# Optimization experiments

Hardware: AMD Instinct MI355X
Metric: run time of the kernel (lower is better)

The kernel has to match this reference:

```python
import jax, jax.numpy as jnp
import numpy as np

N, E, D, H, C, G = 50000, 800000, 128, 128, 16, 512


def setup_inputs() -> dict:
    key = jax.random.key(0)
    ks = jax.random.split(key, 8)

    def glorot(k, shape):
        lim = float(np.sqrt(6.0 / (shape[0] + shape[1])))
        return jax.random.uniform(k, shape, jnp.float32, -lim, lim)

    x = jax.random.normal(ks[0], (N, D), jnp.float32)
    edge_index = jax.random.randint(ks[1], (2, E), 0, N, dtype=jnp.int32)
    batch = jnp.sort(jax.random.randint(ks[2], (N,), 0, G, dtype=jnp.int32))
    return {
        'x': x,
        'edge_index': edge_index,
        'batch': batch,
        'W1': glorot(ks[3], (D, H)), 'b1': jnp.zeros((H,), jnp.float32),
        'W2': glorot(ks[4], (H, H)), 'b2': jnp.zeros((H,), jnp.float32),
        'lW1': glorot(ks[5], (4 * H, 2 * H)), 'lb1': jnp.zeros((2 * H,), jnp.float32),
        'lW2': glorot(ks[6], (2 * H, C)), 'lb2': jnp.zeros((C,), jnp.float32),
    }


def _gcn_norm(edge_index, n):
    # add self loops, then symmetric normalization D^-1/2 (A+I) D^-1/2
    loop = jnp.arange(n, dtype=edge_index.dtype)
    src = jnp.concatenate([edge_index[0], loop])
    dst = jnp.concatenate([edge_index[1], loop])
    ones = jnp.ones(src.shape[0], jnp.float32)
    deg = jax.ops.segment_sum(ones, dst, num_segments=n)
    dis = jnp.where(deg > 0, jax.lax.rsqrt(jnp.maximum(deg, 1.0)), 0.0)
    norm = dis[src] * dis[dst]  # [E+N]
    return src, dst, norm


def _gcn_conv(x, src, dst, norm, W, b, n):
    h = x @ W                                   # [N, H] transform first (PyG order)
    msg = h[src] * norm[:, None]                # gather + normalize, [E+N, H]
    out = jax.ops.segment_sum(msg, dst, num_segments=n)  # scatter-add
    return out + b


def _pool(x, batch, g):
    cnt = jax.ops.segment_sum(jnp.ones(x.shape[0], x.dtype), batch, num_segments=g)
    mean = jax.ops.segment_sum(x, batch, num_segments=g) / jnp.maximum(cnt, 1.0)[:, None]
    mx = jax.ops.segment_max(x, batch, num_segments=g)
    mx = jnp.where(cnt[:, None] > 0, mx, 0.0)
    return mean, mx


def reference(x, edge_index, batch, W1, b1, W2, b2, lW1, lb1, lW2, lb2):
    n = x.shape[0]
    src, dst, norm = _gcn_norm(edge_index, n)
    x0 = jax.nn.relu(_gcn_conv(x, src, dst, norm, W1, b1, n))   # dropout=identity (eval)
    g0_mean, g0_max = _pool(x0, batch, G)
    x1 = jax.nn.relu(_gcn_conv(x0, src, dst, norm, W2, b2, n))
    g1_mean, g1_max = _pool(x1, batch, G)
    g = jnp.concatenate([g0_mean, g0_max, g1_mean, g1_max], axis=-1)  # [G, 4H]
    h = jax.nn.relu(g @ lW1 + lb1)
    return h @ lW2 + lb2  # [G, C]
```

## Files before the change

### kernel.cpp

```cpp
#include <hip/hip_runtime.h>
#include <hip/hip_bf16.h>

#define NN 50000
#define EE 800000
#define DD 128
#define HH 128
#define CC 16
#define GG 512
#define NBLK_SCAN 196
#define NPAD 50176
#define GEMM_BLOCKS 782

typedef __attribute__((ext_vector_type(8))) short short8v;
typedef __attribute__((ext_vector_type(8))) unsigned short ushort8v;
typedef __attribute__((ext_vector_type(4))) float f32x4;

__device__ inline unsigned short f2bf(float x) {
    unsigned int u = __float_as_uint(x);
    u += 0x7fffu + ((u >> 16) & 1u);
    return (unsigned short)(u >> 16);
}

__global__ __launch_bounds__(256) void k_deg(const int* __restrict__ ei, int* __restrict__ deg) {
    int e = blockIdx.x * 256 + threadIdx.x;
    if (e < EE) atomicAdd(&deg[ei[EE + e]], 1);
}

__global__ __launch_bounds__(256) void k_scan1(const int* __restrict__ deg,
                                               int* __restrict__ offs, int* __restrict__ bsum,
                                               float* __restrict__ dis) {
    __shared__ int tmp[256];
    int i = blockIdx.x * 256 + threadIdx.x;
    int v = (i < NN) ? deg[i] : 0;
    if (i < NN) dis[i] = rsqrtf((float)v + 1.0f);
    tmp[threadIdx.x] = v;
    __syncthreads();
    for (int off = 1; off < 256; off <<= 1) {
        int t = (threadIdx.x >= off) ? tmp[threadIdx.x - off] : 0;
        __syncthreads();
        tmp[threadIdx.x] += t;
        __syncthreads();
    }
    if (i < NN) offs[i] = tmp[threadIdx.x] - v;
    if (threadIdx.x == 255) bsum[blockIdx.x] = tmp[255];
}

__global__ __launch_bounds__(256) void k_scan2(int* __restrict__ bsum) {
    __shared__ int tmp[256];
    int v = (threadIdx.x < NBLK_SCAN) ? bsum[threadIdx.x] : 0;
    tmp[threadIdx.x] = v;
    __syncthreads();
    for (int off = 1; off < 256; off <<= 1) {
        int t = (threadIdx.x >= off) ? tmp[threadIdx.x - off] : 0;
        __syncthreads();
        tmp[threadIdx.x] += t;
        __syncthreads();
    }
    bsum[threadIdx.x] = tmp[threadIdx.x] - v;
}

__global__ __launch_bounds__(256) void k_scan3(int* __restrict__ offs, const int* __restrict__ bsum,
                                               int* __restrict__ cursor) {
    int i = blockIdx.x * 256 + threadIdx.x;
    if (i < NN) {
        int v = offs[i] + bsum[blockIdx.x];
        offs[i] = v;
        cursor[i] = v;
    }
}

__global__ __launch_bounds__(256) void k_fill(const int* __restrict__ ei, const float* __restrict__ dis,
                                              int* __restrict__ cursor, unsigned int* __restrict__ adj) {
    int e = blockIdx.x * 256 + threadIdx.x;
    if (e >= EE) return;
    int s = ei[e];
    int d = ei[EE + e];
    int pos = atomicAdd(&cursor[d], 1);
    adj[pos] = ((unsigned int)s << 16) | (unsigned int)f2bf(dis[s] * dis[d]);
}

__global__ __launch_bounds__(256) void k_wfrag(const float* __restrict__ W1, const float* __restrict__ W2,
                                               unsigned short* __restrict__ Wf) {
    const float* W = blockIdx.x ? W2 : W1;
    unsigned short* o = Wf + blockIdx.x * 16384;
    for (int idx = threadIdx.x; idx < 2048; idx += 256) {
        int lane = idx & 63, ct = (idx >> 6) & 7, kt = idx >> 9;
        int col = ct * 16 + (lane & 15);
        int k0 = kt * 32 + (lane >> 4) * 8;
        ushort8v v;
        #pragma unroll
        for (int j = 0; j < 8; ++j) v[j] = f2bf(W[(k0 + j) * 128 + col]);
        *(ushort8v*)(o + idx * 8) = v;
    }
}

__global__ __launch_bounds__(256) void k_gemm(const float* __restrict__ Af,
                                              const unsigned short* __restrict__ Ab,
                                              const unsigned short* __restrict__ Wf,
                                              unsigned short* __restrict__ O,
                                              int af32) {
    __shared__ unsigned short Wl[16384];
    #pragma unroll
    for (int idx = threadIdx.x; idx < 2048; idx += 256)
        *(ushort8v*)(Wl + idx * 8) = *(const ushort8v*)(Wf + idx * 8);
    __syncthreads();

    int wid = threadIdx.x >> 6, lane = threadIdx.x & 63;
    int b = lane >> 4;
    int row = blockIdx.x * 64 + wid * 16 + (lane & 15);

    short8v a[4];
    if (af32) {
        int r = min(row, NN - 1);
        const float* ap = Af + (size_t)r * 128 + b * 8;
        #pragma unroll
        for (int kt = 0; kt < 4; ++kt) {
            float4 f0 = *(const float4*)(ap + kt * 32);
            float4 f1 = *(const float4*)(ap + kt * 32 + 4);
            short8v v;
            v[0] = (short)f2bf(f0.x); v[1] = (short)f2bf(f0.y);
            v[2] = (short)f2bf(f0.z); v[3] = (short)f2bf(f0.w);
            v[4] = (short)f2bf(f1.x); v[5] = (short)f2bf(f1.y);
            v[6] = (short)f2bf(f1.z); v[7] = (short)f2bf(f1.w);
            a[kt] = v;
        }
    } else {
        const unsigned short* ap = Ab + (size_t)row * 128 + b * 8;
        #pragma unroll
        for (int kt = 0; kt < 4; ++kt) a[kt] = *(const short8v*)(ap + kt * 32);
    }

    f32x4 z = 0.0f;
    f32x4 acc[8] = {z, z, z, z, z, z, z, z};
    #pragma unroll
    for (int kt = 0; kt < 4; ++kt) {
        #pragma unroll
        for (int ct = 0; ct < 8; ++ct) {
            short8v bfrag = *(const short8v*)(Wl + ((kt * 8 + ct) * 64 + lane) * 8);
            acc[ct] = __builtin_amdgcn_mfma_f32_16x16x32_bf16(a[kt], bfrag, acc[ct], 0, 0, 0);
        }
    }

    int orow = blockIdx.x * 64 + wid * 16 + b * 4;
    unsigned short* op = O + (size_t)orow * 128 + (lane & 15);
    #pragma unroll
    for (int j = 0; j < 4; ++j) {
        #pragma unroll
        for (int ct = 0; ct < 8; ++ct)
            op[(size_t)j * 128 + ct * 16] = f2bf(acc[ct][j]);
    }
}

__global__ __launch_bounds__(256) void k_conv(const unsigned short* __restrict__ h,
                                              const unsigned int* __restrict__ adj,
                                              const int* __restrict__ row_start,
                                              const int* __restrict__ deg,
                                              const float* __restrict__ dis,
                                              const float* __restrict__ bias,
                                              const int* __restrict__ batch,
                                              unsigned short* __restrict__ xout,
                                              float* __restrict__ gsum,
                                              float* __restrict__ gmax,
                                              float* __restrict__ cnt,
                                              int flags) {
    __shared__ float lacc[16][128];
    __shared__ int lb[16];
    const int tid = threadIdx.x;
    const int wid = tid >> 6, lane = tid & 63;
    const int g = lane >> 4, l = lane & 15;
    const int nrow = wid * 4 + g;
    const int node = blockIdx.x * 16 + nrow;
    const int fb = l * 8;

    const float di = dis[node];
    const float d2 = di * di;
    const uint4 hv = *(const uint4*)(h + (size_t)node * 128 + fb);
    const float4 bv0 = *(const float4*)(bias + fb);
    const float4 bv1 = *(const float4*)(bias + fb + 4);
    float acc[8];
    acc[0] = __uint_as_float(hv.x << 16)         * d2 + bv0.x;
    acc[1] = __uint_as_float(hv.x & 0xffff0000u) * d2 + bv0.y;
    acc[2] = __uint_as_float(hv.y << 16)         * d2 + bv0.z;
    acc[3] = __uint_as_float(hv.y & 0xffff0000u) * d2 + bv0.w;
    acc[4] = __uint_as_float(hv.z << 16)         * d2 + bv1.x;
    acc[5] = __uint_as_float(hv.z & 0xffff0000u) * d2 + bv1.y;
    acc[6] = __uint_as_float(hv.w << 16)         * d2 + bv1.z;
    acc[7] = __uint_as_float(hv.w & 0xffff0000u) * d2 + bv1.w;

    const int rs = row_start[node];
    const int n  = deg[node];
    const unsigned int* ap = adj + rs;
    const int sl = lane & 48;

    for (int k = 0; k < n; k += 16) {
        unsigned int e = ap[min(k + l, n - 1)];
        #pragma unroll
        for (int j = 0; j < 16; ++j) {
            unsigned int ej = __shfl(e, sl + j);
            float w = (k + j < n) ? __uint_as_float(ej << 16) : 0.0f;
            const uint4 v = *(const uint4*)(h + (size_t)(ej >> 16) * 128 + fb);
            acc[0] = fmaf(__uint_as_float(v.x << 16),         w, acc[0]);
            acc[1] = fmaf(__uint_as_float(v.x & 0xffff0000u), w, acc[1]);
            acc[2] = fmaf(__uint_as_float(v.y << 16),         w, acc[2]);
            acc[3] = fmaf(__uint_as_float(v.y & 0xffff0000u), w, acc[3]);
            acc[4] = fmaf(__uint_as_float(v.z << 16),         w, acc[4]);
            acc[5] = fmaf(__uint_as_float(v.z & 0xffff0000u), w, acc[5]);
            acc[6] = fmaf(__uint_as_float(v.w << 16),         w, acc[6]);
            acc[7] = fmaf(__uint_as_float(v.w & 0xffff0000u), w, acc[7]);
        }
    }
    #pragma unroll
    for (int p = 0; p < 8; ++p) acc[p] = fmaxf(acc[p], 0.0f);

    if (flags & 1) {
        uint4 o;
        o.x = (unsigned)f2bf(acc[0]) | ((unsigned)f2bf(acc[1]) << 16);
        o.y = (unsigned)f2bf(acc[2]) | ((unsigned)f2bf(acc[3]) << 16);
        o.z = (unsigned)f2bf(acc[4]) | ((unsigned)f2bf(acc[5]) << 16);
        o.w = (unsigned)f2bf(acc[6]) | ((unsigned)f2bf(acc[7]) << 16);
        *(uint4*)(xout + (size_t)node * 128 + fb) = o;
    }

    #pragma unroll
    for (int p = 0; p < 8; ++p) lacc[nrow][fb + p] = acc[p];
    if (l == 0) lb[nrow] = batch[node];
    __syncthreads();
    {
        const int f = tid & 127;
        const bool domax = tid >= 128;
        float s = lacc[0][f];
        int cur = lb[0], run = 1;
        #pragma unroll
        for (int w = 1; w < 16; ++w) {
            float a = lacc[w][f];
            if (lb[w] == cur) {
                s = domax ? fmaxf(s, a) : (s + a);
                ++run;
            } else {
                if (domax) {
                    atomicMax((int*)&gmax[cur * 128 + f], __float_as_int(s));
                } else {
                    atomicAdd(&gsum[cur * 128 + f], s);
                    if (f == 0 && (flags & 2)) atomicAdd(cnt + cur, (float)run);
                }
                s = a; cur = lb[w]; run = 1;
            }
        }
        if (domax) {
            atomicMax((int*)&gmax[cur * 128 + f], __float_as_int(s));
        } else {
            atomicAdd(&gsum[cur * 128 + f], s);
            if (f == 0 && (flags & 2)) atomicAdd(cnt + cur, (float)run);
        }
    }
}

__global__ __launch_bounds__(256) void k_mlp(const float* __restrict__ gsum0,
                                             const float* __restrict__ gmax0,
                                             const float* __restrict__ gsum1,
                                             const float* __restrict__ gmax1,
                                             const float* __restrict__ cnt,
                                             const float* __restrict__ lW1,
                                             const float* __restrict__ lb1,
                                             const float* __restrict__ lW2,
                                             const float* __restrict__ lb2,
                                             float* __restrict__ out) {
    __shared__ float gl[512];
    __shared__ float hb[256];
    __shared__ float part[256];
    int r = blockIdx.x;
    float inv = 1.0f / fmaxf(cnt[r], 1.0f);
    for (int k = threadIdx.x; k < 512; k += 256) {
        int seg = k >> 7, f = k & 127;
        float v;
        if (seg == 0)      v = gsum0[r * 128 + f] * inv;
        else if (seg == 1) v = gmax0[r * 128 + f];
        else if (seg == 2) v = gsum1[r * 128 + f] * inv;
        else               v = gmax1[r * 128 + f];
        gl[k] = v;
    }
    __syncthreads();
    {
        int j = threadIdx.x;
        float acc = lb1[j];
        for (int k = 0; k < 512; ++k) acc += gl[k] * lW1[k * 256 + j];
        hb[j] = fmaxf(acc, 0.f);
    }
    __syncthreads();
    {
        int c = threadIdx.x & 15, ch = threadIdx.x >> 4;
        float p = 0.f;
        #pragma unroll
        for (int j2 = 0; j2 < 16; ++j2) p += hb[ch * 16 + j2] * lW2[(ch * 16 + j2) * 16 + c];
        part[threadIdx.x] = p;
    }
    __syncthreads();
    if (threadIdx.x < 16) {
        float s = lb2[threadIdx.x];
        #pragma unroll
        for (int ch2 = 0; ch2 < 16; ++ch2) s += part[ch2 * 16 + threadIdx.x];
        out[r * 16 + threadIdx.x] = s;
    }
}

extern "C" void kernel_launch(void* const* d_in, const int* in_sizes, int n_in,
                              void* d_out, int out_size, void* d_ws, size_t ws_size,
                              hipStream_t stream) {
    const float* x    = (const float*)d_in[0];
    const int*   ei   = (const int*)d_in[1];
    const int*   batch= (const int*)d_in[2];
    const float* W1   = (const float*)d_in[3];
    const float* b1   = (const float*)d_in[4];
    const float* W2   = (const float*)d_in[5];
    const float* b2   = (const float*)d_in[6];
    const float* lW1  = (const float*)d_in[7];
    const float* lb1  = (const float*)d_in[8];
    const float* lW2  = (const float*)d_in[9];
    const float* lb2  = (const float*)d_in[10];
    float* out = (float*)d_out;

    unsigned short* hbuf = (unsigned short*)d_ws;
    unsigned short* x0b  = hbuf + (size_t)NPAD * 128;
    unsigned short* wf   = x0b + (size_t)NPAD * 128;
    float* dis   = (float*)(wf + 32768);
    float* gsum0 = dis + NPAD;
    float* gmax0 = gsum0 + GG * HH;
    float* gsum1 = gmax0 + GG * HH;
    float* gmax1 = gsum1 + GG * HH;
    float* cnt   = gmax1 + GG * HH;
    int*   deg    = (int*)(cnt + GG);
    int*   offs   = deg + NPAD;
    int*   cursor = offs + NPAD;
    int*   bsum   = cursor + NPAD;
    unsigned int* adj = (unsigned int*)(bsum + 256);

    hipMemsetAsync(deg, 0, NPAD * sizeof(int), stream);
    k_deg<<<(EE + 255) / 256, 256, 0, stream>>>(ei, deg);
    k_scan1<<<NBLK_SCAN, 256, 0, stream>>>(deg, offs, bsum, dis);
    k_scan2<<<1, 256, 0, stream>>>(bsum);
    k_scan3<<<NBLK_SCAN, 256, 0, stream>>>(offs, bsum, cursor);
    k_fill<<<(EE + 255) / 256, 256, 0, stream>>>(ei, dis, cursor, adj);

    k_wfrag<<<2, 256, 0, stream>>>(W1, W2, wf);
    hipMemsetAsync(gsum0, 0, (size_t)(4 * GG * HH + GG) * sizeof(float), stream);

    k_gemm<<<GEMM_BLOCKS, 256, 0, stream>>>(x, (const unsigned short*)nullptr, wf, hbuf, 1);
    k_conv<<<NN / 16, 256, 0, stream>>>(hbuf, adj, offs, deg, dis, b1, batch,
                                        x0b, gsum0, gmax0, cnt, 3);
    k_gemm<<<GEMM_BLOCKS, 256, 0, stream>>>((const float*)nullptr, x0b, wf + 16384, hbuf, 0);
    k_conv<<<NN / 16, 256, 0, stream>>>(hbuf, adj, offs, deg, dis, b2, batch,
                                        x0b, gsum1, gmax1, cnt, 0);

    k_mlp<<<GG, 256, 0, stream>>>(gsum0, gmax0, gsum1, gmax1, cnt, lW1, lb1, lW2, lb2, out);
}
```

Before: 210.8 us.

## Fuse init memsets and weight packing into one kernel; batch edge fill; peel conv tail

Replaces the two hipMemsetAsync calls and the weight-fragment kernel with a single grid-stride init kernel, which cuts launch count. The CSR fill kernel now handles four edges per thread so several atomics and gathers are in flight at once. The conv loop splits into full 16-edge chunks with no bounds predicate plus one masked tail chunk. The atomic fill order within a row can change, so floating-point summation order may differ.

```diff
diff --git a/kernel.cpp b/kernel.cpp
--- a/kernel.cpp
+++ b/kernel.cpp
@@ -10,6 +10,8 @@
 #define NBLK_SCAN 196
 #define NPAD 50176
 #define GEMM_BLOCKS 782
+#define POOLF (4 * GG * HH + GG)
+#define EQ 200000
 
 typedef __attribute__((ext_vector_type(8))) short short8v;
 typedef __attribute__((ext_vector_type(8))) unsigned short ushort8v;
@@ -19,6 +21,26 @@
     unsigned int u = __float_as_uint(x);
     u += 0x7fffu + ((u >> 16) & 1u);
     return (unsigned short)(u >> 16);
+}
+
+__global__ __launch_bounds__(256) void k_init(const float* __restrict__ W1, const float* __restrict__ W2,
+                                              unsigned short* __restrict__ Wf,
+                                              int* __restrict__ deg, float* __restrict__ pools) {
+    int tid = blockIdx.x * 256 + threadIdx.x;
+    int nt = gridDim.x * 256;
+    for (int i = tid; i < NPAD; i += nt) deg[i] = 0;
+    for (int i = tid; i < POOLF; i += nt) pools[i] = 0.0f;
+    for (int idx = tid; idx < 4096; idx += nt) {
+        const float* W = (idx >> 11) ? W2 : W1;
+        int id2 = idx & 2047;
+        int lane = id2 & 63, ct = (id2 >> 6) & 7, kt = id2 >> 9;
+        int col = ct * 16 + (lane & 15);
+        int k0 = kt * 32 + (lane >> 4) * 8;
+        ushort8v v;
+        #pragma unroll
+        for (int j = 0; j < 8; ++j) v[j] = f2bf(W[(k0 + j) * 128 + col]);
+        *(ushort8v*)(Wf + idx * 8) = v;
+    }
 }
 
 __global__ __launch_bounds__(256) void k_deg(const int* __restrict__ ei, int* __restrict__ deg) {
@@ -71,27 +93,24 @@
 
 __global__ __launch_bounds__(256) void k_fill(const int* __restrict__ ei, const float* __restrict__ dis,
                                               int* __restrict__ cursor, unsigned int* __restrict__ adj) {
-    int e = blockIdx.x * 256 + threadIdx.x;
-    if (e >= EE) return;
-    int s = ei[e];
-    int d = ei[EE + e];
-    int pos = atomicAdd(&cursor[d], 1);
-    adj[pos] = ((unsigned int)s << 16) | (unsigned int)f2bf(dis[s] * dis[d]);
-}
-
-__global__ __launch_bounds__(256) void k_wfrag(const float* __restrict__ W1, const float* __restrict__ W2,
-                                               unsigned short* __restrict__ Wf) {
-    const float* W = blockIdx.x ? W2 : W1;
-    unsigned short* o = Wf + blockIdx.x * 16384;
-    for (int idx = threadIdx.x; idx < 2048; idx += 256) {
-        int lane = idx & 63, ct = (idx >> 6) & 7, kt = idx >> 9;
-        int col = ct * 16 + (lane & 15);
-        int k0 = kt * 32 + (lane >> 4) * 8;
-        ushort8v v;
-        #pragma unroll
-        for (int j = 0; j < 8; ++j) v[j] = f2bf(W[(k0 + j) * 128 + col]);
-        *(ushort8v*)(o + idx * 8) = v;
-    }
+    int base = blockIdx.x * 256 + threadIdx.x;
+    if (base >= EQ) return;
+    int s0 = ei[base];            int d0 = ei[EE + base];
+    int s1 = ei[base + EQ];       int d1 = ei[EE + base + EQ];
+    int s2 = ei[base + 2 * EQ];   int d2 = ei[EE + base + 2 * EQ];
+    int s3 = ei[base + 3 * EQ];   int d3 = ei[EE + base + 3 * EQ];
+    float n0 = dis[s0] * dis[d0];
+    float n1 = dis[s1] * dis[d1];
+    float n2 = dis[s2] * dis[d2];
+    float n3 = dis[s3] * dis[d3];
+    int p0 = atomicAdd(&cursor[d0], 1);
+    int p1 = atomicAdd(&cursor[d1], 1);
+    int p2 = atomicAdd(&cursor[d2], 1);
+    int p3 = atomicAdd(&cursor[d3], 1);
+    adj[p0] = ((unsigned int)s0 << 16) | (unsigned int)f2bf(n0);
+    adj[p1] = ((unsigned int)s1 << 16) | (unsigned int)f2bf(n1);
+    adj[p2] = ((unsigned int)s2 << 16) | (unsigned int)f2bf(n2);
+    adj[p3] = ((unsigned int)s3 << 16) | (unsigned int)f2bf(n3);
 }
 
 __global__ __launch_bounds__(256) void k_gemm(const float* __restrict__ Af,
@@ -191,13 +210,31 @@
     const int n  = deg[node];
     const unsigned int* ap = adj + rs;
     const int sl = lane & 48;
-
-    for (int k = 0; k < n; k += 16) {
-        unsigned int e = ap[min(k + l, n - 1)];
+    const int nfull = n & ~15;
+
+    for (int k = 0; k < nfull; k += 16) {
+        unsigned int e = ap[k + l];
         #pragma unroll
         for (int j = 0; j < 16; ++j) {
             unsigned int ej = __shfl(e, sl + j);
-            float w = (k + j < n) ? __uint_as_float(ej << 16) : 0.0f;
+            float w = __uint_as_float(ej << 16);
+            const uint4 v = *(const uint4*)(h + (size_t)(ej >> 16) * 128 + fb);
+            acc[0] = fmaf(__uint_as_float(v.x << 16),         w, acc[0]);
+            acc[1] = fmaf(__uint_as_float(v.x & 0xffff0000u), w, acc[1]);
+            acc[2] = fmaf(__uint_as_float(v.y << 16),         w, acc[2]);
+            acc[3] = fmaf(__uint_as_float(v.y & 0xffff0000u), w, acc[3]);
+            acc[4] = fmaf(__uint_as_float(v.z << 16),         w, acc[4]);
+            acc[5] = fmaf(__uint_as_float(v.z & 0xffff0000u), w, acc[5]);
+            acc[6] = fmaf(__uint_as_float(v.w << 16),         w, acc[6]);
+            acc[7] = fmaf(__uint_as_float(v.w & 0xffff0000u), w, acc[7]);
+        }
+    }
+    if (nfull < n) {
+        unsigned int e = ap[min(nfull + l, n - 1)];
+        #pragma unroll
+        for (int j = 0; j < 16; ++j) {
+            unsigned int ej = __shfl(e, sl + j);
+            float w = (nfull + j < n) ? __uint_as_float(ej << 16) : 0.0f;
             const uint4 v = *(const uint4*)(h + (size_t)(ej >> 16) * 128 + fb);
             acc[0] = fmaf(__uint_as_float(v.x << 16),         w, acc[0]);
             acc[1] = fmaf(__uint_as_float(v.x & 0xffff0000u), w, acc[1]);
@@ -334,15 +371,13 @@
     int*   bsum   = cursor + NPAD;
     unsigned int* adj = (unsigned int*)(bsum + 256);
 
-    hipMemsetAsync(deg, 0, NPAD * sizeof(int), stream);
+    k_init<<<256, 256, 0, stream>>>(W1, W2, wf, deg, gsum0);
+
     k_deg<<<(EE + 255) / 256, 256, 0, stream>>>(ei, deg);
     k_scan1<<<NBLK_SCAN, 256, 0, stream>>>(deg, offs, bsum, dis);
     k_scan2<<<1, 256, 0, stream>>>(bsum);
     k_scan3<<<NBLK_SCAN, 256, 0, stream>>>(offs, bsum, cursor);
-    k_fill<<<(EE + 255) / 256, 256, 0, stream>>>(ei, dis, cursor, adj);
-
-    k_wfrag<<<2, 256, 0, stream>>>(W1, W2, wf);
-    hipMemsetAsync(gsum0, 0, (size_t)(4 * GG * HH + GG) * sizeof(float), stream);
+    k_fill<<<(EQ + 255) / 256, 256, 0, stream>>>(ei, dis, cursor, adj);
 
     k_gemm<<<GEMM_BLOCKS, 256, 0, stream>>>(x, (const unsigned short*)nullptr, wf, hbuf, 1);
     k_conv<<<NN / 16, 256, 0, stream>>>(hbuf, adj, offs, deg, dis, b1, batch,
```

After: 219.8 us. 4.3% more time.
